# Performance work log

Measured on AMD Instinct MI355X. Metric: run time of the kernel, lower is better.

The kernel has to match this reference:

```python
import jax, jax.numpy as jnp
import numpy as np
import math

NUM_HEADS = 8

def setup_inputs() -> dict:
    key = jax.random.key(0)
    ks = jax.random.split(key, 5)
    b, h, w, c = 4, 128, 128, 256
    x = jax.random.normal(ks[0], (b, h, w, c), dtype=jnp.float32)
    scale = 1.0 / math.sqrt(c)  # keep weights reasonably scaled (kaiming-like)
    Wq = jax.random.normal(ks[1], (c, c), dtype=jnp.float32) * scale
    Wk = jax.random.normal(ks[2], (c, c), dtype=jnp.float32) * scale
    Wv = jax.random.normal(ks[3], (c, c), dtype=jnp.float32) * scale
    Wout = jax.random.normal(ks[4], (c, c), dtype=jnp.float32) * scale
    return {"x": x, "Wq": Wq, "Wk": Wk, "Wv": Wv, "Wout": Wout}

def reference(x, Wq, Wk, Wv, Wout):
    b, h, w, c = x.shape
    hw = h * w
    heads = NUM_HEADS
    dh = c // heads
    xs = x.reshape(b, hw, c)
    q = xs @ Wq  # (b, hw, c)
    k = xs @ Wk
    v = xs @ Wv

    def split_heads(t):
        # (b, hw, c) -> (b, c, hw) -> (b, heads, dh, hw)
        return t.transpose(0, 2, 1).reshape(b, heads, dh, hw)

    q = split_heads(q)
    k = split_heads(k)
    v = split_heads(v)
    # L2-normalize along the feature (hw) axis; original has no epsilon
    q = q / jnp.linalg.norm(q, axis=-1, keepdims=True)
    k = k / jnp.linalg.norm(k, axis=-1, keepdims=True)
    d_k = q.shape[-1]  # = hw
    attn = jnp.einsum('bhcd,bhed->bhce', q, k) / math.sqrt(d_k)  # (b,heads,dh,dh)
    attn = jax.nn.softmax(attn, axis=-1)
    vals = jnp.einsum('bhce,bhed->bhcd', attn, v)  # (b,heads,dh,hw)
    vals = vals.transpose(0, 3, 1, 2).reshape(b, hw, c)
    out = (vals @ Wout).reshape(b, h, w, c)
    return out
```

## Files before the change

kernel.cpp:

```cpp
#include <hip/hip_runtime.h>


#define B_   4
#define HW_  16384
#define C_   256

typedef __attribute__((ext_vector_type(8))) short short8;
typedef __attribute__((ext_vector_type(4))) float floatx4;

__device__ __forceinline__ unsigned short f2bf(float f) {
  unsigned u = __builtin_bit_cast(unsigned, f);
  u += 0x7FFFu + ((u >> 16) & 1u);
  return (unsigned short)(u >> 16);
}

__device__ __forceinline__ void gl_lds16(const unsigned short* g, unsigned short* l) {
  __builtin_amdgcn_global_load_lds(
      (const __attribute__((address_space(1))) unsigned int*)g,
      (__attribute__((address_space(3))) unsigned int*)l, 16, 0, 0);
}

__global__ __launch_bounds__(512) void k_sgemm(const float* __restrict__ x,
                                               float* __restrict__ part) {
  __shared__ unsigned short Pt[256 * 128];
  int bid = blockIdx.x;
  int ks = bid & 31, b = bid >> 5;
  const float* xv = x + ((size_t)(b * HW_ + ks * 512)) * C_;
  int t = threadIdx.x, lane = t & 63, w = t >> 6;
  int wq = w >> 1, hh = w & 1;
  int wm = wq >> 1, wn = wq & 1;
  int l15 = lane & 15, l4 = lane >> 4;
  int s_cq  = (lane >> 3) | (w << 3);
  int s_hpl = lane & 7;
  floatx4 acc[4][8];
  floatx4 z = {0.f, 0.f, 0.f, 0.f};
#pragma unroll
  for (int i = 0; i < 4; i++)
#pragma unroll
    for (int j = 0; j < 8; j++) acc[i][j] = z;

  for (int ph = 0; ph < 4; ph++) {
    if (ph) __syncthreads();
#pragma unroll
    for (int e = 0; e < 8; e++) {
      int hp = s_hpl | (e << 3);
      int hw = hp * 2;
      const float* src = xv + ((size_t)(ph * 128 + hw)) * C_ + s_cq * 4;
      float4 v0 = *(const float4*)src;
      float4 v1 = *(const float4*)(src + C_);
      float a0[4] = {v0.x, v0.y, v0.z, v0.w};
      float a1[4] = {v1.x, v1.y, v1.z, v1.w};
#pragma unroll
      for (int i = 0; i < 4; i++) {
        unsigned u = (unsigned)f2bf(a0[i]) | ((unsigned)f2bf(a1[i]) << 16);
        int r = s_cq * 4 + i;
        int slot = (hp >> 2) ^ (r & 15);
        ((unsigned*)Pt)[r * 64 + slot * 4 + (hp & 3)] = u;
      }
    }
    __syncthreads();
#pragma unroll
    for (int kk = 0; kk < 4; kk++) {
      short8 af[4], bfv[8];
      int oct = kk * 4 + l4;
#pragma unroll
      for (int tm = 0; tm < 4; tm++) {
        int row = wm * 128 + hh * 64 + tm * 16 + l15;
        af[tm] = *(const short8*)(Pt + row * 128 + ((oct ^ (row & 15)) * 8));
      }
#pragma unroll
      for (int tn = 0; tn < 8; tn++) {
        int row = wn * 128 + tn * 16 + l15;
        bfv[tn] = *(const short8*)(Pt + row * 128 + ((oct ^ (row & 15)) * 8));
      }
#pragma unroll
      for (int tm = 0; tm < 4; tm++)
#pragma unroll
        for (int tn = 0; tn < 8; tn++)
          acc[tm][tn] = __builtin_amdgcn_mfma_f32_16x16x32_bf16(af[tm], bfv[tn],
                                                                acc[tm][tn], 0, 0, 0);
    }
  }
  float* pb = part + (size_t)(b * 32 + ks) * 65536;
#pragma unroll
  for (int tm = 0; tm < 4; tm++)
#pragma unroll
    for (int tn = 0; tn < 8; tn++)
#pragma unroll
      for (int r = 0; r < 4; r++) {
        int m = wm * 128 + hh * 64 + tm * 16 + l4 * 4 + r;
        int n = wn * 128 + tn * 16 + l15;
        pb[m * 256 + n] = acc[tm][tn][r];
      }
}

__global__ __launch_bounds__(256) void k_sred(const float* __restrict__ part,
                                              float* __restrict__ S) {
  int idx = blockIdx.x * 256 + threadIdx.x;
  int b = idx >> 16;
  int mn = idx & 65535;
  const float* p = part + ((size_t)b << 21) + mn;
  float s = 0.f;
#pragma unroll
  for (int k = 0; k < 32; k++) s += p[(size_t)k << 16];
  S[idx] = s;
}

__global__ __launch_bounds__(256) void k_gemm_sw(const float* __restrict__ S,
                                                 const float* __restrict__ Wq,
                                                 const float* __restrict__ Wk,
                                                 float* __restrict__ SWq,
                                                 float* __restrict__ SWk) {
  __shared__ float Ast[16][68];
  __shared__ float Bs[16][68];
  int bid = blockIdx.x;
  int nt = bid & 7, mt = (bid >> 3) & 3, b = bid >> 5;
  int mb = mt * 64;
  const float* Wsel = (nt < 4) ? Wq : Wk;
  int nb = (nt & 3) * 64;
  int t = threadIdx.x, tx = t & 15, ty = t >> 4;
  float acc[4][4] = {};
  for (int kt = 0; kt < 16; kt++) {
    {
      int row = t >> 2, kq = t & 3;
      float4 v = *(const float4*)(S + ((size_t)(b * C_ + mb + row)) * C_ + kt * 16 + kq * 4);
      Ast[kq * 4 + 0][row] = v.x; Ast[kq * 4 + 1][row] = v.y;
      Ast[kq * 4 + 2][row] = v.z; Ast[kq * 4 + 3][row] = v.w;
    }
    {
      int kk = t >> 4, n4 = t & 15;
      float4 v = *(const float4*)(Wsel + ((size_t)(kt * 16 + kk)) * C_ + nb + n4 * 4);
      *(float4*)&Bs[kk][n4 * 4] = v;
    }
    __syncthreads();
#pragma unroll
    for (int k = 0; k < 16; k++) {
      float4 a4 = *(const float4*)&Ast[k][ty * 4];
      float4 b4 = *(const float4*)&Bs[k][tx * 4];
      float a[4] = {a4.x, a4.y, a4.z, a4.w};
      float bb[4] = {b4.x, b4.y, b4.z, b4.w};
#pragma unroll
      for (int i = 0; i < 4; i++)
#pragma unroll
        for (int j = 0; j < 4; j++) acc[i][j] += a[i] * bb[j];
    }
    __syncthreads();
  }
#pragma unroll
  for (int i = 0; i < 4; i++)
#pragma unroll
    for (int j = 0; j < 4; j++) {
      int row = mb + ty * 4 + i;
      int ng = nt * 64 + tx * 4 + j;
      if (ng < 256) SWq[((size_t)(b * C_ + row)) * C_ + ng] = acc[i][j];
      else          SWk[((size_t)(b * C_ + row)) * C_ + ng - 256] = acc[i][j];
    }
}

__global__ __launch_bounds__(256) void k_fuse(const float* __restrict__ Wq,
                                              const float* __restrict__ Wk,
                                              const float* __restrict__ SWq,
                                              const float* __restrict__ SWk,
                                              const float* __restrict__ Wout,
                                              float* __restrict__ U) {
  __shared__ float Wqh[256][32];
  __shared__ float Wkh[256][32];
  __shared__ float SWqh[256][32];
  __shared__ float SWkh[256][32];
  __shared__ float Lg[32][33];
  __shared__ float qp[8][32], kp[8][32], qin[32], kin[32];
  int b = blockIdx.x >> 3, h = blockIdx.x & 7;
  int t = threadIdx.x;
  int col = t & 31, rgrp = t >> 5;
  for (int r0 = 0; r0 < 256; r0 += 8) {
    int row = r0 + rgrp;
    Wqh[row][col]  = Wq[(size_t)row * C_ + h * 32 + col];
    Wkh[row][col]  = Wk[(size_t)row * C_ + h * 32 + col];
    SWqh[row][col] = SWq[((size_t)(b * C_ + row)) * C_ + h * 32 + col];
    SWkh[row][col] = SWk[((size_t)(b * C_ + row)) * C_ + h * 32 + col];
  }
  __syncthreads();
  {
    float g[4] = {0.f, 0.f, 0.f, 0.f};
    for (int k = 0; k < 256; k++) {
      float swk = SWkh[k][col];
#pragma unroll
      for (int r = 0; r < 4; r++) g[r] += Wqh[k][rgrp + 8 * r] * swk;
    }
#pragma unroll
    for (int r = 0; r < 4; r++) Lg[rgrp + 8 * r][col] = g[r];
  }
  {
    float sq = 0.f, sk = 0.f;
    for (int k = rgrp * 32; k < rgrp * 32 + 32; k++) {
      sq += Wqh[k][col] * SWqh[k][col];
      sk += Wkh[k][col] * SWkh[k][col];
    }
    qp[rgrp][col] = sq;
    kp[rgrp][col] = sk;
  }
  __syncthreads();
  if (t < 32) {
    float a = 0.f;
#pragma unroll
    for (int p = 0; p < 8; p++) a += qp[p][t];
    qin[t] = rsqrtf(a);
  } else if (t < 64) {
    int j = t - 32;
    float a = 0.f;
#pragma unroll
    for (int p = 0; p < 8; p++) a += kp[p][j];
    kin[j] = rsqrtf(a);
  }
  __syncthreads();
  if (t < 32) {
    float row[32];
    float mx = -1e30f;
#pragma unroll
    for (int j = 0; j < 32; j++) {
      row[j] = Lg[t][j] * qin[t] * kin[j] * 0.0078125f;
      mx = fmaxf(mx, row[j]);
    }
    float sum = 0.f;
#pragma unroll
    for (int j = 0; j < 32; j++) { row[j] = __expf(row[j] - mx); sum += row[j]; }
    float inv = 1.0f / sum;
#pragma unroll
    for (int j = 0; j < 32; j++) Lg[t][j] = row[j] * inv;
  }
  __syncthreads();
  float (*Wo)[256] = reinterpret_cast<float(*)[256]>(&Wqh[0][0]);
#pragma unroll
  for (int r = 0; r < 32; r++) Wo[r][t] = Wout[((size_t)(h * 32 + r)) * C_ + t];
  __syncthreads();
  for (int j = 0; j < 32; j++) {
    float a = 0.f;
#pragma unroll
    for (int i2 = 0; i2 < 32; i2++) a += Lg[i2][j] * Wo[i2][t];
    U[((size_t)(b * C_ + h * 32 + j)) * C_ + t] = a;
  }
}

__global__ __launch_bounds__(256) void k_gemm_w3(const float* __restrict__ Wv,
                                                 const float* __restrict__ U,
                                                 unsigned short* __restrict__ W3bT) {
  __shared__ float Ast[16][68];
  __shared__ float Bs[16][68];
  int bid = blockIdx.x;
  int nt = bid & 3, mt = (bid >> 2) & 3, b = bid >> 4;
  int mb = mt * 64, nb = nt * 64;
  int t = threadIdx.x, tx = t & 15, ty = t >> 4;
  float acc[4][4] = {};
  for (int kt = 0; kt < 16; kt++) {
    {
      int row = t >> 2, kq = t & 3;
      float4 v = *(const float4*)(Wv + ((size_t)(mb + row)) * C_ + kt * 16 + kq * 4);
      Ast[kq * 4 + 0][row] = v.x; Ast[kq * 4 + 1][row] = v.y;
      Ast[kq * 4 + 2][row] = v.z; Ast[kq * 4 + 3][row] = v.w;
    }
    {
      int kk = t >> 4, n4 = t & 15;
      float4 v = *(const float4*)(U + ((size_t)(b * C_ + kt * 16 + kk)) * C_ + nb + n4 * 4);
      *(float4*)&Bs[kk][n4 * 4] = v;
    }
    __syncthreads();
#pragma unroll
    for (int k = 0; k < 16; k++) {
      float4 a4 = *(const float4*)&Ast[k][ty * 4];
      float4 b4 = *(const float4*)&Bs[k][tx * 4];
      float a[4] = {a4.x, a4.y, a4.z, a4.w};
      float bb[4] = {b4.x, b4.y, b4.z, b4.w};
#pragma unroll
      for (int i = 0; i < 4; i++)
#pragma unroll
        for (int j = 0; j < 4; j++) acc[i][j] += a[i] * bb[j];
    }
    __syncthreads();
  }
#pragma unroll
  for (int i = 0; i < 4; i++)
#pragma unroll
    for (int j = 0; j < 4; j++)
      W3bT[((size_t)(b * C_ + nb + tx * 4 + j)) * C_ + mb + ty * 4 + i] = f2bf(acc[i][j]);
}

__global__ __launch_bounds__(256) void k_out(const float* __restrict__ x,
                                             const unsigned short* __restrict__ W3bT,
                                             float* __restrict__ out) {
  __shared__ unsigned short Bt[256 * 64];
  int mtile = blockIdx.x;
  int b = mtile >> 7;
  const float* Ax = x + (size_t)mtile * 128 * C_;
  const unsigned short* Bb = W3bT + (size_t)b * C_ * C_;
  int t = threadIdx.x, lane = t & 63, w = t >> 6;
  int hf = w >> 1, c2 = w & 1;
  int l8 = lane >> 3, l7 = lane & 7;
  int srcoct = l7 ^ l8;
  int l15 = lane & 15, l4 = lane >> 4;
  floatx4 acc[4][8];
  floatx4 z = {0.f, 0.f, 0.f, 0.f};
#pragma unroll
  for (int i = 0; i < 4; i++)
#pragma unroll
    for (int j = 0; j < 8; j++) acc[i][j] = z;
  for (int s = 0; s < 4; s++) {
    if (s) __syncthreads();
#pragma unroll
    for (int i = 0; i < 8; i++) {
      int ib = w * 8 + i;
      int row = ib * 8 + l8;
      gl_lds16(Bb + (size_t)row * C_ + s * 64 + srcoct * 8, Bt + ib * 512);
    }
    __syncthreads();
#pragma unroll
    for (int kk = 0; kk < 2; kk++) {
      short8 af[4], bfv[8];
      int oct = kk * 4 + l4;
#pragma unroll
      for (int tm = 0; tm < 4; tm++) {
        int row = hf * 64 + tm * 16 + l15;
        const float* p = Ax + (size_t)row * C_ + s * 64 + oct * 8;
        float4 u0 = *(const float4*)p;
        float4 u1 = *(const float4*)(p + 4);
        short8 v;
        v[0] = (short)f2bf(u0.x); v[1] = (short)f2bf(u0.y);
        v[2] = (short)f2bf(u0.z); v[3] = (short)f2bf(u0.w);
        v[4] = (short)f2bf(u1.x); v[5] = (short)f2bf(u1.y);
        v[6] = (short)f2bf(u1.z); v[7] = (short)f2bf(u1.w);
        af[tm] = v;
      }
#pragma unroll
      for (int tn = 0; tn < 8; tn++) {
        int row = c2 * 128 + tn * 16 + l15;
        bfv[tn] = *(const short8*)(Bt + row * 64 + ((oct ^ (row & 7)) * 8));
      }
#pragma unroll
      for (int tm = 0; tm < 4; tm++)
#pragma unroll
        for (int tn = 0; tn < 8; tn++)
          acc[tm][tn] = __builtin_amdgcn_mfma_f32_16x16x32_bf16(af[tm], bfv[tn],
                                                                acc[tm][tn], 0, 0, 0);
    }
  }
  float* ob = out + (size_t)mtile * 128 * C_;
#pragma unroll
  for (int tm = 0; tm < 4; tm++)
#pragma unroll
    for (int tn = 0; tn < 8; tn++)
#pragma unroll
      for (int r = 0; r < 4; r++) {
        int m = hf * 64 + tm * 16 + l4 * 4 + r;
        int n = c2 * 128 + tn * 16 + l15;
        ob[(size_t)m * C_ + n] = acc[tm][tn][r];
      }
}

extern "C" void kernel_launch(void* const* d_in, const int* in_sizes, int n_in,
                              void* d_out, int out_size, void* d_ws, size_t ws_size,
                              hipStream_t stream) {
  const float* x    = (const float*)d_in[0];
  const float* Wq   = (const float*)d_in[1];
  const float* Wk   = (const float*)d_in[2];
  const float* Wv   = (const float*)d_in[3];
  const float* Wout = (const float*)d_in[4];
  float* out = (float*)d_out;

  float* part = (float*)d_ws;
  float* S    = part + (size_t)8388608;
  float* SWq  = S + 262144;
  float* SWk  = SWq + 262144;
  float* U    = SWk + 262144;
  unsigned short* W3bT = (unsigned short*)(U + 262144);

  k_sgemm<<<dim3(128), dim3(512), 0, stream>>>(x, part);
  k_sred<<<dim3(1024), dim3(256), 0, stream>>>(part, S);
  k_gemm_sw<<<dim3(128), dim3(256), 0, stream>>>(S, Wq, Wk, SWq, SWk);
  k_fuse<<<dim3(32), dim3(256), 0, stream>>>(Wq, Wk, SWq, SWk, Wout, U);
  k_gemm_w3<<<dim3(64), dim3(256), 0, stream>>>(Wv, U, W3bT);
  k_out<<<dim3(512), dim3(256), 0, stream>>>(x, W3bT, out);
}
```

Before: 218.9 us.

## Merge small middle kernels into one grid-barrier kernel and split sgemm across more blocks

```diff
diff --git a/kernel.cpp b/kernel.cpp
--- a/kernel.cpp
+++ b/kernel.cpp
@@ -20,268 +20,311 @@
       (__attribute__((address_space(3))) unsigned int*)l, 16, 0, 0);
 }
 
+__device__ __forceinline__ void gridbar(unsigned* c) {
+  __syncthreads();
+  if (threadIdx.x == 0) {
+    __hip_atomic_fetch_add(c, 1u, __ATOMIC_RELEASE, __HIP_MEMORY_SCOPE_AGENT);
+    for (int spin = 0; spin < (1 << 24); ++spin) {
+      if (__hip_atomic_load(c, __ATOMIC_ACQUIRE, __HIP_MEMORY_SCOPE_AGENT) >= 256u) break;
+      __builtin_amdgcn_s_sleep(8);
+    }
+  }
+  __syncthreads();
+}
+
 __global__ __launch_bounds__(512) void k_sgemm(const float* __restrict__ x,
-                                               float* __restrict__ part) {
+                                               float* __restrict__ part,
+                                               unsigned* __restrict__ bars) {
+  if (blockIdx.x == 0 && threadIdx.x < 8)
+    __hip_atomic_store(bars + threadIdx.x, 0u, __ATOMIC_RELAXED, __HIP_MEMORY_SCOPE_AGENT);
   __shared__ unsigned short Pt[256 * 128];
   int bid = blockIdx.x;
-  int ks = bid & 31, b = bid >> 5;
+  int hs = bid & 1, ks = (bid >> 1) & 31, b = bid >> 6;
   const float* xv = x + ((size_t)(b * HW_ + ks * 512)) * C_;
   int t = threadIdx.x, lane = t & 63, w = t >> 6;
-  int wq = w >> 1, hh = w & 1;
-  int wm = wq >> 1, wn = wq & 1;
+  int rw = w >> 2, cw = w & 3;
+  int m0 = hs * 128 + rw * 64;
+  int n0 = cw * 64;
   int l15 = lane & 15, l4 = lane >> 4;
   int s_cq  = (lane >> 3) | (w << 3);
   int s_hpl = lane & 7;
-  floatx4 acc[4][8];
+  floatx4 acc[4][4];
   floatx4 z = {0.f, 0.f, 0.f, 0.f};
 #pragma unroll
   for (int i = 0; i < 4; i++)
 #pragma unroll
-    for (int j = 0; j < 8; j++) acc[i][j] = z;
-
+    for (int j = 0; j < 4; j++) acc[i][j] = z;
+
+#pragma unroll
+  for (int e = 0; e < 8; e++) {
+    int hp = s_hpl | (e << 3);
+    const float* src = xv + ((size_t)(hp * 2)) * C_ + s_cq * 4;
+    float4 v0 = *(const float4*)src;
+    float4 v1 = *(const float4*)(src + C_);
+    float a0[4] = {v0.x, v0.y, v0.z, v0.w};
+    float a1[4] = {v1.x, v1.y, v1.z, v1.w};
+#pragma unroll
+    for (int i = 0; i < 4; i++) {
+      unsigned u = (unsigned)f2bf(a0[i]) | ((unsigned)f2bf(a1[i]) << 16);
+      int r = s_cq * 4 + i;
+      int slot = (hp >> 2) ^ (r & 15);
+      ((unsigned*)Pt)[r * 64 + slot * 4 + (hp & 3)] = u;
+    }
+  }
+  __syncthreads();
+
+  float4 pA[8], pB[8];
   for (int ph = 0; ph < 4; ph++) {
-    if (ph) __syncthreads();
-#pragma unroll
-    for (int e = 0; e < 8; e++) {
-      int hp = s_hpl | (e << 3);
-      int hw = hp * 2;
-      const float* src = xv + ((size_t)(ph * 128 + hw)) * C_ + s_cq * 4;
-      float4 v0 = *(const float4*)src;
-      float4 v1 = *(const float4*)(src + C_);
-      float a0[4] = {v0.x, v0.y, v0.z, v0.w};
-      float a1[4] = {v1.x, v1.y, v1.z, v1.w};
-#pragma unroll
-      for (int i = 0; i < 4; i++) {
-        unsigned u = (unsigned)f2bf(a0[i]) | ((unsigned)f2bf(a1[i]) << 16);
-        int r = s_cq * 4 + i;
-        int slot = (hp >> 2) ^ (r & 15);
-        ((unsigned*)Pt)[r * 64 + slot * 4 + (hp & 3)] = u;
-      }
-    }
-    __syncthreads();
+    if (ph < 3) {
+#pragma unroll
+      for (int e = 0; e < 8; e++) {
+        int hp = s_hpl | (e << 3);
+        const float* src = xv + ((size_t)((ph + 1) * 128 + hp * 2)) * C_ + s_cq * 4;
+        pA[e] = *(const float4*)src;
+        pB[e] = *(const float4*)(src + C_);
+      }
+    }
 #pragma unroll
     for (int kk = 0; kk < 4; kk++) {
-      short8 af[4], bfv[8];
+      short8 af[4], bfv[4];
       int oct = kk * 4 + l4;
 #pragma unroll
       for (int tm = 0; tm < 4; tm++) {
-        int row = wm * 128 + hh * 64 + tm * 16 + l15;
+        int row = m0 + tm * 16 + l15;
         af[tm] = *(const short8*)(Pt + row * 128 + ((oct ^ (row & 15)) * 8));
       }
 #pragma unroll
-      for (int tn = 0; tn < 8; tn++) {
-        int row = wn * 128 + tn * 16 + l15;
+      for (int tn = 0; tn < 4; tn++) {
+        int row = n0 + tn * 16 + l15;
         bfv[tn] = *(const short8*)(Pt + row * 128 + ((oct ^ (row & 15)) * 8));
       }
 #pragma unroll
       for (int tm = 0; tm < 4; tm++)
 #pragma unroll
-        for (int tn = 0; tn < 8; tn++)
+        for (int tn = 0; tn < 4; tn++)
           acc[tm][tn] = __builtin_amdgcn_mfma_f32_16x16x32_bf16(af[tm], bfv[tn],
                                                                 acc[tm][tn], 0, 0, 0);
     }
+    if (ph < 3) {
+      __syncthreads();
+#pragma unroll
+      for (int e = 0; e < 8; e++) {
+        int hp = s_hpl | (e << 3);
+        float a0[4] = {pA[e].x, pA[e].y, pA[e].z, pA[e].w};
+        float a1[4] = {pB[e].x, pB[e].y, pB[e].z, pB[e].w};
+#pragma unroll
+        for (int i = 0; i < 4; i++) {
+          unsigned u = (unsigned)f2bf(a0[i]) | ((unsigned)f2bf(a1[i]) << 16);
+          int r = s_cq * 4 + i;
+          int slot = (hp >> 2) ^ (r & 15);
+          ((unsigned*)Pt)[r * 64 + slot * 4 + (hp & 3)] = u;
+        }
+      }
+      __syncthreads();
+    }
   }
   float* pb = part + (size_t)(b * 32 + ks) * 65536;
 #pragma unroll
   for (int tm = 0; tm < 4; tm++)
 #pragma unroll
-    for (int tn = 0; tn < 8; tn++)
+    for (int tn = 0; tn < 4; tn++)
 #pragma unroll
       for (int r = 0; r < 4; r++) {
-        int m = wm * 128 + hh * 64 + tm * 16 + l4 * 4 + r;
-        int n = wn * 128 + tn * 16 + l15;
+        int m = m0 + tm * 16 + l4 * 4 + r;
+        int n = n0 + tn * 16 + l15;
         pb[m * 256 + n] = acc[tm][tn][r];
       }
 }
 
-__global__ __launch_bounds__(256) void k_sred(const float* __restrict__ part,
-                                              float* __restrict__ S) {
-  int idx = blockIdx.x * 256 + threadIdx.x;
-  int b = idx >> 16;
-  int mn = idx & 65535;
-  const float* p = part + ((size_t)b << 21) + mn;
-  float s = 0.f;
-#pragma unroll
-  for (int k = 0; k < 32; k++) s += p[(size_t)k << 16];
-  S[idx] = s;
-}
-
-__global__ __launch_bounds__(256) void k_gemm_sw(const float* __restrict__ S,
-                                                 const float* __restrict__ Wq,
-                                                 const float* __restrict__ Wk,
-                                                 float* __restrict__ SWq,
-                                                 float* __restrict__ SWk) {
-  __shared__ float Ast[16][68];
-  __shared__ float Bs[16][68];
-  int bid = blockIdx.x;
-  int nt = bid & 7, mt = (bid >> 3) & 3, b = bid >> 5;
-  int mb = mt * 64;
-  const float* Wsel = (nt < 4) ? Wq : Wk;
-  int nb = (nt & 3) * 64;
-  int t = threadIdx.x, tx = t & 15, ty = t >> 4;
-  float acc[4][4] = {};
-  for (int kt = 0; kt < 16; kt++) {
+__global__ __launch_bounds__(256) void k_mega(const float* __restrict__ part,
+                                              float* __restrict__ S,
+                                              const float* __restrict__ Wq,
+                                              const float* __restrict__ Wk,
+                                              float* __restrict__ SWq,
+                                              float* __restrict__ SWk,
+                                              const float* __restrict__ Wout,
+                                              const float* __restrict__ Wv,
+                                              float* __restrict__ U,
+                                              unsigned short* __restrict__ W3bT,
+                                              unsigned* __restrict__ bars) {
+  __shared__ union {
+    struct { float Ast[16][68]; float Bs[16][68]; } g;
+    struct { float Wqh[256][32]; float Wkh[256][32];
+             float SWqh[256][32]; float SWkh[256][32];
+             float Lg[32][33]; float qp[8][32]; float kp[8][32];
+             float qin[32]; float kin[32]; } f;
+  } sh;
+  int bid = blockIdx.x, t = threadIdx.x;
+
+  {
+    int g = bid * 256 + t;
+    int b = g >> 14, off = (g & 16383) * 4;
+    const float* p = part + ((size_t)b << 21) + off;
+    float4 s = {0.f, 0.f, 0.f, 0.f};
+#pragma unroll
+    for (int k = 0; k < 32; k++) {
+      float4 v = *(const float4*)(p + ((size_t)k << 16));
+      s.x += v.x; s.y += v.y; s.z += v.z; s.w += v.w;
+    }
+    *(float4*)(S + ((size_t)b << 16) + off) = s;
+  }
+  gridbar(bars + 0);
+
+  if (bid < 128) {
+    int nt = bid & 7, mt = (bid >> 3) & 3, b = bid >> 5;
+    int mb = mt * 64;
+    const float* Wsel = (nt < 4) ? Wq : Wk;
+    int nb = (nt & 3) * 64;
+    int tx = t & 15, ty = t >> 4;
+    float acc[4][4] = {};
+    for (int kt = 0; kt < 16; kt++) {
+      {
+        int row = t >> 2, kq = t & 3;
+        float4 v = *(const float4*)(S + ((size_t)(b * C_ + mb + row)) * C_ + kt * 16 + kq * 4);
+        sh.g.Ast[kq * 4 + 0][row] = v.x; sh.g.Ast[kq * 4 + 1][row] = v.y;
+        sh.g.Ast[kq * 4 + 2][row] = v.z; sh.g.Ast[kq * 4 + 3][row] = v.w;
+      }
+      {
+        int kk = t >> 4, n4 = t & 15;
+        float4 v = *(const float4*)(Wsel + ((size_t)(kt * 16 + kk)) * C_ + nb + n4 * 4);
+        *(float4*)&sh.g.Bs[kk][n4 * 4] = v;
+      }
+      __syncthreads();
+#pragma unroll
+      for (int k = 0; k < 16; k++) {
+        float4 a4 = *(const float4*)&sh.g.Ast[k][ty * 4];
+        float4 b4 = *(const float4*)&sh.g.Bs[k][tx * 4];
+        float a[4] = {a4.x, a4.y, a4.z, a4.w};
+        float bb[4] = {b4.x, b4.y, b4.z, b4.w};
+#pragma unroll
+        for (int i = 0; i < 4; i++)
+#pragma unroll
+          for (int j = 0; j < 4; j++) acc[i][j] += a[i] * bb[j];
+      }
+      __syncthreads();
+    }
+#pragma unroll
+    for (int i = 0; i < 4; i++)
+#pragma unroll
+      for (int j = 0; j < 4; j++) {
+        int row = mb + ty * 4 + i;
+        int ng = nt * 64 + tx * 4 + j;
+        if (ng < 256) SWq[((size_t)(b * C_ + row)) * C_ + ng] = acc[i][j];
+        else          SWk[((size_t)(b * C_ + row)) * C_ + ng - 256] = acc[i][j];
+      }
+  }
+  gridbar(bars + 1);
+
+  if (bid < 32) {
+    int b = bid >> 3, h = bid & 7;
+    int col = t & 31, rgrp = t >> 5;
+    for (int r0 = 0; r0 < 256; r0 += 8) {
+      int row = r0 + rgrp;
+      sh.f.Wqh[row][col]  = Wq[(size_t)row * C_ + h * 32 + col];
+      sh.f.Wkh[row][col]  = Wk[(size_t)row * C_ + h * 32 + col];
+      sh.f.SWqh[row][col] = SWq[((size_t)(b * C_ + row)) * C_ + h * 32 + col];
+      sh.f.SWkh[row][col] = SWk[((size_t)(b * C_ + row)) * C_ + h * 32 + col];
+    }
+    __syncthreads();
     {
-      int row = t >> 2, kq = t & 3;
-      float4 v = *(const float4*)(S + ((size_t)(b * C_ + mb + row)) * C_ + kt * 16 + kq * 4);
-      Ast[kq * 4 + 0][row] = v.x; Ast[kq * 4 + 1][row] = v.y;
-      Ast[kq * 4 + 2][row] = v.z; Ast[kq * 4 + 3][row] = v.w;
+      float g[4] = {0.f, 0.f, 0.f, 0.f};
+      for (int k = 0; k < 256; k++) {
+        float swk = sh.f.SWkh[k][col];
+#pragma unroll
+        for (int r = 0; r < 4; r++) g[r] += sh.f.Wqh[k][rgrp + 8 * r] * swk;
+      }
+#pragma unroll
+      for (int r = 0; r < 4; r++) sh.f.Lg[rgrp + 8 * r][col] = g[r];
     }
     {
-      int kk = t >> 4, n4 = t & 15;
-      float4 v = *(const float4*)(Wsel + ((size_t)(kt * 16 + kk)) * C_ + nb + n4 * 4);
-      *(float4*)&Bs[kk][n4 * 4] = v;
-    }
-    __syncthreads();
-#pragma unroll
-    for (int k = 0; k < 16; k++) {
-      float4 a4 = *(const float4*)&Ast[k][ty * 4];
-      float4 b4 = *(const float4*)&Bs[k][tx * 4];
-      float a[4] = {a4.x, a4.y, a4.z, a4.w};
-      float bb[4] = {b4.x, b4.y, b4.z, b4.w};
-#pragma unroll
-      for (int i = 0; i < 4; i++)
-#pragma unroll
-        for (int j = 0; j < 4; j++) acc[i][j] += a[i] * bb[j];
-    }
-    __syncthreads();
-  }
-#pragma unroll
-  for (int i = 0; i < 4; i++)
-#pragma unroll
-    for (int j = 0; j < 4; j++) {
-      int row = mb + ty * 4 + i;
-      int ng = nt * 64 + tx * 4 + j;
-      if (ng < 256) SWq[((size_t)(b * C_ + row)) * C_ + ng] = acc[i][j];
-      else          SWk[((size_t)(b * C_ + row)) * C_ + ng - 256] = acc[i][j];
-    }
-}
-
-__global__ __launch_bounds__(256) void k_fuse(const float* __restrict__ Wq,
-                                              const float* __restrict__ Wk,
-                                              const float* __restrict__ SWq,
-                                              const float* __restrict__ SWk,
-                                              const float* __restrict__ Wout,
-                                              float* __restrict__ U) {
-  __shared__ float Wqh[256][32];
-  __shared__ float Wkh[256][32];
-  __shared__ float SWqh[256][32];
-  __shared__ float SWkh[256][32];
-  __shared__ float Lg[32][33];
-  __shared__ float qp[8][32], kp[8][32], qin[32], kin[32];
-  int b = blockIdx.x >> 3, h = blockIdx.x & 7;
-  int t = threadIdx.x;
-  int col = t & 31, rgrp = t >> 5;
-  for (int r0 = 0; r0 < 256; r0 += 8) {
-    int row = r0 + rgrp;
-    Wqh[row][col]  = Wq[(size_t)row * C_ + h * 32 + col];
-    Wkh[row][col]  = Wk[(size_t)row * C_ + h * 32 + col];
-    SWqh[row][col] = SWq[((size_t)(b * C_ + row)) * C_ + h * 32 + col];
-    SWkh[row][col] = SWk[((size_t)(b * C_ + row)) * C_ + h * 32 + col];
-  }
-  __syncthreads();
-  {
-    float g[4] = {0.f, 0.f, 0.f, 0.f};
-    for (int k = 0; k < 256; k++) {
-      float swk = SWkh[k][col];
-#pragma unroll
-      for (int r = 0; r < 4; r++) g[r] += Wqh[k][rgrp + 8 * r] * swk;
-    }
-#pragma unroll
-    for (int r = 0; r < 4; r++) Lg[rgrp + 8 * r][col] = g[r];
-  }
-  {
-    float sq = 0.f, sk = 0.f;
-    for (int k = rgrp * 32; k < rgrp * 32 + 32; k++) {
-      sq += Wqh[k][col] * SWqh[k][col];
-      sk += Wkh[k][col] * SWkh[k][col];
-    }
-    qp[rgrp][col] = sq;
-    kp[rgrp][col] = sk;
-  }
-  __syncthreads();
-  if (t < 32) {
-    float a = 0.f;
-#pragma unroll
-    for (int p = 0; p < 8; p++) a += qp[p][t];
-    qin[t] = rsqrtf(a);
-  } else if (t < 64) {
-    int j = t - 32;
-    float a = 0.f;
-#pragma unroll
-    for (int p = 0; p < 8; p++) a += kp[p][j];
-    kin[j] = rsqrtf(a);
-  }
-  __syncthreads();
-  if (t < 32) {
-    float row[32];
-    float mx = -1e30f;
-#pragma unroll
+      float sq = 0.f, sk = 0.f;
+      for (int k = rgrp * 32; k < rgrp * 32 + 32; k++) {
+        sq += sh.f.Wqh[k][col] * sh.f.SWqh[k][col];
+        sk += sh.f.Wkh[k][col] * sh.f.SWkh[k][col];
+      }
+      sh.f.qp[rgrp][col] = sq;
+      sh.f.kp[rgrp][col] = sk;
+    }
+    __syncthreads();
+    if (t < 32) {
+      float a = 0.f;
+#pragma unroll
+      for (int p = 0; p < 8; p++) a += sh.f.qp[p][t];
+      sh.f.qin[t] = rsqrtf(a);
+    } else if (t < 64) {
+      int j = t - 32;
+      float a = 0.f;
+#pragma unroll
+      for (int p = 0; p < 8; p++) a += sh.f.kp[p][j];
+      sh.f.kin[j] = rsqrtf(a);
+    }
+    __syncthreads();
+    if (t < 32) {
+      float row[32];
+      float mx = -1e30f;
+#pragma unroll
+      for (int j = 0; j < 32; j++) {
+        row[j] = sh.f.Lg[t][j] * sh.f.qin[t] * sh.f.kin[j] * 0.0078125f;
+        mx = fmaxf(mx, row[j]);
+      }
+      float sum = 0.f;
+#pragma unroll
+      for (int j = 0; j < 32; j++) { row[j] = __expf(row[j] - mx); sum += row[j]; }
+      float inv = 1.0f / sum;
+#pragma unroll
+      for (int j = 0; j < 32; j++) sh.f.Lg[t][j] = row[j] * inv;
+    }
+    __syncthreads();
+    float (*Wo)[256] = reinterpret_cast<float(*)[256]>(&sh.f.Wqh[0][0]);
+#pragma unroll
+    for (int r = 0; r < 32; r++) Wo[r][t] = Wout[((size_t)(h * 32 + r)) * C_ + t];
+    __syncthreads();
     for (int j = 0; j < 32; j++) {
-      row[j] = Lg[t][j] * qin[t] * kin[j] * 0.0078125f;
-      mx = fmaxf(mx, row[j]);
-    }
-    float sum = 0.f;
-#pragma unroll
-    for (int j = 0; j < 32; j++) { row[j] = __expf(row[j] - mx); sum += row[j]; }
-    float inv = 1.0f / sum;
-#pragma unroll
-    for (int j = 0; j < 32; j++) Lg[t][j] = row[j] * inv;
-  }
-  __syncthreads();
-  float (*Wo)[256] = reinterpret_cast<float(*)[256]>(&Wqh[0][0]);
-#pragma unroll
-  for (int r = 0; r < 32; r++) Wo[r][t] = Wout[((size_t)(h * 32 + r)) * C_ + t];
-  __syncthreads();
-  for (int j = 0; j < 32; j++) {
-    float a = 0.f;
-#pragma unroll
-    for (int i2 = 0; i2 < 32; i2++) a += Lg[i2][j] * Wo[i2][t];
-    U[((size_t)(b * C_ + h * 32 + j)) * C_ + t] = a;
-  }
-}
-
-__global__ __launch_bounds__(256) void k_gemm_w3(const float* __restrict__ Wv,
-                                                 const float* __restrict__ U,
-                                                 unsigned short* __restrict__ W3bT) {
-  __shared__ float Ast[16][68];
-  __shared__ float Bs[16][68];
-  int bid = blockIdx.x;
-  int nt = bid & 3, mt = (bid >> 2) & 3, b = bid >> 4;
-  int mb = mt * 64, nb = nt * 64;
-  int t = threadIdx.x, tx = t & 15, ty = t >> 4;
-  float acc[4][4] = {};
-  for (int kt = 0; kt < 16; kt++) {
-    {
-      int row = t >> 2, kq = t & 3;
-      float4 v = *(const float4*)(Wv + ((size_t)(mb + row)) * C_ + kt * 16 + kq * 4);
-      Ast[kq * 4 + 0][row] = v.x; Ast[kq * 4 + 1][row] = v.y;
-      Ast[kq * 4 + 2][row] = v.z; Ast[kq * 4 + 3][row] = v.w;
-    }
-    {
-      int kk = t >> 4, n4 = t & 15;
-      float4 v = *(const float4*)(U + ((size_t)(b * C_ + kt * 16 + kk)) * C_ + nb + n4 * 4);
-      *(float4*)&Bs[kk][n4 * 4] = v;
-    }
-    __syncthreads();
-#pragma unroll
-    for (int k = 0; k < 16; k++) {
-      float4 a4 = *(const float4*)&Ast[k][ty * 4];
-      float4 b4 = *(const float4*)&Bs[k][tx * 4];
-      float a[4] = {a4.x, a4.y, a4.z, a4.w};
-      float bb[4] = {b4.x, b4.y, b4.z, b4.w};
-#pragma unroll
-      for (int i = 0; i < 4; i++)
-#pragma unroll
-        for (int j = 0; j < 4; j++) acc[i][j] += a[i] * bb[j];
-    }
-    __syncthreads();
-  }
-#pragma unroll
-  for (int i = 0; i < 4; i++)
-#pragma unroll
-    for (int j = 0; j < 4; j++)
-      W3bT[((size_t)(b * C_ + nb + tx * 4 + j)) * C_ + mb + ty * 4 + i] = f2bf(acc[i][j]);
+      float a = 0.f;
+#pragma unroll
+      for (int i2 = 0; i2 < 32; i2++) a += sh.f.Lg[i2][j] * Wo[i2][t];
+      U[((size_t)(b * C_ + h * 32 + j)) * C_ + t] = a;
+    }
+  }
+  gridbar(bars + 2);
+
+  if (bid < 64) {
+    int nt = bid & 3, mt = (bid >> 2) & 3, b = bid >> 4;
+    int mb = mt * 64, nb = nt * 64;
+    int tx = t & 15, ty = t >> 4;
+    float acc[4][4] = {};
+    for (int kt = 0; kt < 16; kt++) {
+      {
+        int row = t >> 2, kq = t & 3;
+        float4 v = *(const float4*)(Wv + ((size_t)(mb + row)) * C_ + kt * 16 + kq * 4);
+        sh.g.Ast[kq * 4 + 0][row] = v.x; sh.g.Ast[kq * 4 + 1][row] = v.y;
+        sh.g.Ast[kq * 4 + 2][row] = v.z; sh.g.Ast[kq * 4 + 3][row] = v.w;
+      }
+      {
+        int kk = t >> 4, n4 = t & 15;
+        float4 v = *(const float4*)(U + ((size_t)(b * C_ + kt * 16 + kk)) * C_ + nb + n4 * 4);
+        *(float4*)&sh.g.Bs[kk][n4 * 4] = v;
+      }
+      __syncthreads();
+#pragma unroll
+      for (int k = 0; k < 16; k++) {
+        float4 a4 = *(const float4*)&sh.g.Ast[k][ty * 4];
+        float4 b4 = *(const float4*)&sh.g.Bs[k][tx * 4];
+        float a[4] = {a4.x, a4.y, a4.z, a4.w};
+        float bb[4] = {b4.x, b4.y, b4.z, b4.w};
+#pragma unroll
+        for (int i = 0; i < 4; i++)
+#pragma unroll
+          for (int j = 0; j < 4; j++) acc[i][j] += a[i] * bb[j];
+      }
+      __syncthreads();
+    }
+#pragma unroll
+    for (int i = 0; i < 4; i++)
+#pragma unroll
+      for (int j = 0; j < 4; j++)
+        W3bT[((size_t)(b * C_ + nb + tx * 4 + j)) * C_ + mb + ty * 4 + i] = f2bf(acc[i][j]);
+  }
 }
 
 __global__ __launch_bounds__(256) void k_out(const float* __restrict__ x,
@@ -371,11 +414,10 @@
   float* SWk  = SWq + 262144;
   float* U    = SWk + 262144;
   unsigned short* W3bT = (unsigned short*)(U + 262144);
-
-  k_sgemm<<<dim3(128), dim3(512), 0, stream>>>(x, part);
-  k_sred<<<dim3(1024), dim3(256), 0, stream>>>(part, S);
-  k_gemm_sw<<<dim3(128), dim3(256), 0, stream>>>(S, Wq, Wk, SWq, SWk);
-  k_fuse<<<dim3(32), dim3(256), 0, stream>>>(Wq, Wk, SWq, SWk, Wout, U);
-  k_gemm_w3<<<dim3(64), dim3(256), 0, stream>>>(Wv, U, W3bT);
+  unsigned* bars = (unsigned*)(W3bT + 262144);
+
+  k_sgemm<<<dim3(256), dim3(512), 0, stream>>>(x, part, bars);
+  k_mega<<<dim3(256), dim3(256), 0, stream>>>(part, S, Wq, Wk, SWq, SWk,
+                                              Wout, Wv, U, W3bT, bars);
   k_out<<<dim3(512), dim3(256), 0, stream>>>(x, W3bT, out);
 }
```

Measured after the change: 292.4 us. 1.34x slower.

## Split Gram GEMM output across two blocks, prefetch next x chunk, vectorize reduction

Applied to the files above, without the earlier changes.

```diff
diff --git a/kernel.cpp b/kernel.cpp
--- a/kernel.cpp
+++ b/kernel.cpp
@@ -24,86 +24,115 @@
                                                float* __restrict__ part) {
   __shared__ unsigned short Pt[256 * 128];
   int bid = blockIdx.x;
-  int ks = bid & 31, b = bid >> 5;
+  int hs = bid & 1, ks = (bid >> 1) & 31, b = bid >> 6;
   const float* xv = x + ((size_t)(b * HW_ + ks * 512)) * C_;
   int t = threadIdx.x, lane = t & 63, w = t >> 6;
-  int wq = w >> 1, hh = w & 1;
-  int wm = wq >> 1, wn = wq & 1;
+  int rw = w >> 2, cw = w & 3;
+  int m0 = hs * 128 + rw * 64;
+  int n0 = cw * 64;
   int l15 = lane & 15, l4 = lane >> 4;
   int s_cq  = (lane >> 3) | (w << 3);
   int s_hpl = lane & 7;
-  floatx4 acc[4][8];
+  floatx4 acc[4][4];
   floatx4 z = {0.f, 0.f, 0.f, 0.f};
 #pragma unroll
   for (int i = 0; i < 4; i++)
 #pragma unroll
-    for (int j = 0; j < 8; j++) acc[i][j] = z;
-
+    for (int j = 0; j < 4; j++) acc[i][j] = z;
+
+#pragma unroll
+  for (int e = 0; e < 8; e++) {
+    int hp = s_hpl | (e << 3);
+    const float* src = xv + ((size_t)(hp * 2)) * C_ + s_cq * 4;
+    float4 v0 = *(const float4*)src;
+    float4 v1 = *(const float4*)(src + C_);
+    float a0[4] = {v0.x, v0.y, v0.z, v0.w};
+    float a1[4] = {v1.x, v1.y, v1.z, v1.w};
+#pragma unroll
+    for (int i = 0; i < 4; i++) {
+      unsigned u = (unsigned)f2bf(a0[i]) | ((unsigned)f2bf(a1[i]) << 16);
+      int r = s_cq * 4 + i;
+      int slot = (hp >> 2) ^ (r & 15);
+      ((unsigned*)Pt)[r * 64 + slot * 4 + (hp & 3)] = u;
+    }
+  }
+  __syncthreads();
+
+  float4 pA[8], pB[8];
   for (int ph = 0; ph < 4; ph++) {
-    if (ph) __syncthreads();
-#pragma unroll
-    for (int e = 0; e < 8; e++) {
-      int hp = s_hpl | (e << 3);
-      int hw = hp * 2;
-      const float* src = xv + ((size_t)(ph * 128 + hw)) * C_ + s_cq * 4;
-      float4 v0 = *(const float4*)src;
-      float4 v1 = *(const float4*)(src + C_);
-      float a0[4] = {v0.x, v0.y, v0.z, v0.w};
-      float a1[4] = {v1.x, v1.y, v1.z, v1.w};
-#pragma unroll
-      for (int i = 0; i < 4; i++) {
-        unsigned u = (unsigned)f2bf(a0[i]) | ((unsigned)f2bf(a1[i]) << 16);
-        int r = s_cq * 4 + i;
-        int slot = (hp >> 2) ^ (r & 15);
-        ((unsigned*)Pt)[r * 64 + slot * 4 + (hp & 3)] = u;
-      }
-    }
-    __syncthreads();
+    if (ph < 3) {
+#pragma unroll
+      for (int e = 0; e < 8; e++) {
+        int hp = s_hpl | (e << 3);
+        const float* src = xv + ((size_t)((ph + 1) * 128 + hp * 2)) * C_ + s_cq * 4;
+        pA[e] = *(const float4*)src;
+        pB[e] = *(const float4*)(src + C_);
+      }
+    }
 #pragma unroll
     for (int kk = 0; kk < 4; kk++) {
-      short8 af[4], bfv[8];
+      short8 af[4], bfv[4];
       int oct = kk * 4 + l4;
 #pragma unroll
       for (int tm = 0; tm < 4; tm++) {
-        int row = wm * 128 + hh * 64 + tm * 16 + l15;
+        int row = m0 + tm * 16 + l15;
         af[tm] = *(const short8*)(Pt + row * 128 + ((oct ^ (row & 15)) * 8));
       }
 #pragma unroll
-      for (int tn = 0; tn < 8; tn++) {
-        int row = wn * 128 + tn * 16 + l15;
+      for (int tn = 0; tn < 4; tn++) {
+        int row = n0 + tn * 16 + l15;
         bfv[tn] = *(const short8*)(Pt + row * 128 + ((oct ^ (row & 15)) * 8));
       }
 #pragma unroll
       for (int tm = 0; tm < 4; tm++)
 #pragma unroll
-        for (int tn = 0; tn < 8; tn++)
+        for (int tn = 0; tn < 4; tn++)
           acc[tm][tn] = __builtin_amdgcn_mfma_f32_16x16x32_bf16(af[tm], bfv[tn],
                                                                 acc[tm][tn], 0, 0, 0);
     }
+    if (ph < 3) {
+      __syncthreads();
+#pragma unroll
+      for (int e = 0; e < 8; e++) {
+        int hp = s_hpl | (e << 3);
+        float a0[4] = {pA[e].x, pA[e].y, pA[e].z, pA[e].w};
+        float a1[4] = {pB[e].x, pB[e].y, pB[e].z, pB[e].w};
+#pragma unroll
+        for (int i = 0; i < 4; i++) {
+          unsigned u = (unsigned)f2bf(a0[i]) | ((unsigned)f2bf(a1[i]) << 16);
+          int r = s_cq * 4 + i;
+          int slot = (hp >> 2) ^ (r & 15);
+          ((unsigned*)Pt)[r * 64 + slot * 4 + (hp & 3)] = u;
+        }
+      }
+      __syncthreads();
+    }
   }
   float* pb = part + (size_t)(b * 32 + ks) * 65536;
 #pragma unroll
   for (int tm = 0; tm < 4; tm++)
 #pragma unroll
-    for (int tn = 0; tn < 8; tn++)
+    for (int tn = 0; tn < 4; tn++)
 #pragma unroll
       for (int r = 0; r < 4; r++) {
-        int m = wm * 128 + hh * 64 + tm * 16 + l4 * 4 + r;
-        int n = wn * 128 + tn * 16 + l15;
+        int m = m0 + tm * 16 + l4 * 4 + r;
+        int n = n0 + tn * 16 + l15;
         pb[m * 256 + n] = acc[tm][tn][r];
       }
 }
 
 __global__ __launch_bounds__(256) void k_sred(const float* __restrict__ part,
                                               float* __restrict__ S) {
-  int idx = blockIdx.x * 256 + threadIdx.x;
-  int b = idx >> 16;
-  int mn = idx & 65535;
-  const float* p = part + ((size_t)b << 21) + mn;
-  float s = 0.f;
-#pragma unroll
-  for (int k = 0; k < 32; k++) s += p[(size_t)k << 16];
-  S[idx] = s;
+  int g = blockIdx.x * 256 + threadIdx.x;
+  int b = g >> 14, off = (g & 16383) * 4;
+  const float* p = part + ((size_t)b << 21) + off;
+  float4 s = {0.f, 0.f, 0.f, 0.f};
+#pragma unroll
+  for (int k = 0; k < 32; k++) {
+    float4 v = *(const float4*)(p + ((size_t)k << 16));
+    s.x += v.x; s.y += v.y; s.z += v.z; s.w += v.w;
+  }
+  *(float4*)(S + ((size_t)b << 16) + off) = s;
 }
 
 __global__ __launch_bounds__(256) void k_gemm_sw(const float* __restrict__ S,
@@ -372,8 +401,8 @@
   float* U    = SWk + 262144;
   unsigned short* W3bT = (unsigned short*)(U + 262144);
 
-  k_sgemm<<<dim3(128), dim3(512), 0, stream>>>(x, part);
-  k_sred<<<dim3(1024), dim3(256), 0, stream>>>(part, S);
+  k_sgemm<<<dim3(256), dim3(512), 0, stream>>>(x, part);
+  k_sred<<<dim3(256), dim3(256), 0, stream>>>(part, S);
   k_gemm_sw<<<dim3(128), dim3(256), 0, stream>>>(S, Wq, Wk, SWq, SWk);
   k_fuse<<<dim3(32), dim3(256), 0, stream>>>(Wq, Wk, SWq, SWk, Wout, U);
   k_gemm_w3<<<dim3(64), dim3(256), 0, stream>>>(Wv, U, W3bT);
```

New measurement: 219.9 us. Within noise of the previous version (+0.4%).
